# Optimization experiments

Measured on AMD Instinct MI355X. Metric: run time of the kernel, lower is better.

Reference implementation:

```python
import jax, jax.numpy as jnp
import numpy as np

B, C, T = 2, 128, 25000
OUT_C = 128
N_NODES = B * T            # 50000, nodes after flatten
N_EDGES = 800000           # avg degree 16


def setup_inputs() -> dict:
    key = jax.random.key(0)
    k1, k2, k3 = jax.random.split(key, 3)
    x = jax.random.normal(k1, (B, C, T), dtype=jnp.float32)
    W = jax.random.normal(k2, (C, OUT_C), dtype=jnp.float32) * (1.0 / np.sqrt(C))
    bias = jnp.zeros((OUT_C,), dtype=jnp.float32)
    edge_index = jax.random.randint(k3, (2, N_EDGES), 0, N_NODES, dtype=jnp.int64)
    return {"x": x, "W": W, "bias": bias, "edge_index": edge_index}


def reference(x, W, bias, edge_index):
    b, c, t = x.shape
    n = b * t
    flat = x.transpose(0, 2, 1).reshape(n, c)          # [N, C]
    h = flat @ W                                       # [N, OUT_C] transform first (GCNConv)
    src, dst = edge_index[0], edge_index[1]
    # in-degree with self-loops (PyG GCNConv default symmetric norm)
    deg = jnp.zeros((n,), dtype=h.dtype).at[dst].add(1.0) + 1.0
    dinv_sqrt = jax.lax.rsqrt(deg)
    norm = dinv_sqrt[src] * dinv_sqrt[dst]             # [E]
    msgs = h[src] * norm[:, None]                      # [E, OUT_C] gather + scale
    agg = jax.ops.segment_sum(msgs, dst, num_segments=n)
    agg = agg + h * (1.0 / deg)[:, None]               # self-loop term: norm_ii = 1/deg_i
    out = jax.nn.relu(agg + bias)
    return out.reshape(b, t, -1).transpose(0, 2, 1)    # [B, OUT_C, T]
```

## Files before the change

kernel.cpp:

```cpp
#include <hip/hip_runtime.h>

#define TT 25000
#define BB 2
#define CC 128
#define NN (BB*TT)
#define NB ((NN + 255) / 256)

typedef __attribute__((ext_vector_type(8))) short bf16x8;
typedef __attribute__((ext_vector_type(4))) float f32x4;

__device__ inline unsigned short f2bf(float f) {
    unsigned int u = __float_as_uint(f);
    u += 0x7FFF + ((u >> 16) & 1);
    return (unsigned short)(u >> 16);
}
__device__ inline float bfhi(unsigned int v) { return __uint_as_float(v << 16); }
__device__ inline float bflo(unsigned int v) { return __uint_as_float(v & 0xFFFF0000u); }

__global__ __launch_bounds__(256) void k_deg(const int* __restrict__ dst, int E,
                                             int* __restrict__ deg,
                                             int* __restrict__ eseq) {
    int i0 = blockIdx.x * 512 + threadIdx.x;
    int i1 = i0 + 256;
    int d0 = 0, d1 = 0;
    bool ok0 = (i0 < E), ok1 = (i1 < E);
    if (ok0) d0 = dst[i0];
    if (ok1) d1 = dst[i1];
    if (ok0) eseq[i0] = atomicAdd(&deg[d0], 1);
    if (ok1) eseq[i1] = atomicAdd(&deg[d1], 1);
}

__global__ __launch_bounds__(256) void k_bsum(const int* __restrict__ deg,
                                              int* __restrict__ bsum) {
    __shared__ int red[256];
    int tid = threadIdx.x;
    int i = blockIdx.x * 256 + tid;
    red[tid] = (i < NN) ? deg[i] : 0;
    __syncthreads();
#pragma unroll
    for (int o = 128; o > 0; o >>= 1) {
        if (tid < o) red[tid] += red[tid + o];
        __syncthreads();
    }
    if (tid == 0) bsum[blockIdx.x] = red[0];
}

__global__ __launch_bounds__(256) void k_scan2(const int* __restrict__ deg,
                                               const int* __restrict__ bsum,
                                               int* __restrict__ off,
                                               float* __restrict__ dinv) {
    __shared__ int part[256];
    __shared__ int bpref;
    int tid = threadIdx.x;
    int i = blockIdx.x * 256 + tid;

    part[tid] = (tid < NB && tid < blockIdx.x) ? bsum[tid] : 0;
    __syncthreads();
#pragma unroll
    for (int o = 128; o > 0; o >>= 1) {
        if (tid < o) part[tid] += part[tid + o];
        __syncthreads();
    }
    if (tid == 0) bpref = part[0];
    __syncthreads();
    int base = bpref;
    __syncthreads();

    int v = (i < NN) ? deg[i] : 0;
    part[tid] = v;
    __syncthreads();
#pragma unroll
    for (int o = 1; o < 256; o <<= 1) {
        int u = (tid >= o) ? part[tid - o] : 0;
        __syncthreads();
        part[tid] += u;
        __syncthreads();
    }
    int incl = part[tid];
    if (i < NN) {
        off[i]  = base + incl - v;
        dinv[i] = rsqrtf((float)(v + 1));
    }
    if (i == NN - 1) off[NN] = base + incl;
}

__global__ __launch_bounds__(256) void k_fill(const int* __restrict__ src,
                                              const int* __restrict__ dst, int E,
                                              const int* __restrict__ off,
                                              const int* __restrict__ eseq,
                                              int* __restrict__ csr_src) {
    int i = blockIdx.x * blockDim.x + threadIdx.x;
    if (i < E) {
        int d = dst[i];
        csr_src[off[d] + eseq[i]] = src[i];
    }
}

__global__ __launch_bounds__(256) void k_gemm(const float* __restrict__ x,
                                              const float* __restrict__ W,
                                              const float* __restrict__ dinv,
                                              unsigned short* __restrict__ h) {
    __shared__ __align__(16) unsigned short a_lds[4][4][64][8];
    __shared__ __align__(16) unsigned short b_lds[8][4][64][8];
    int tid = threadIdx.x;
    int n0 = blockIdx.x * 64;

    {
        int m = tid & 63;
        int n = n0 + m;
        bool ok = (n < NN);
        int b = 0, t = 0;
        if (ok) { b = n / TT; t = n - b * TT; }
        const float* xp = x + ((size_t)b * CC) * TT + t;
        int mt = m >> 4, lm = m & 15;
#pragma unroll
        for (int p = 0; p < 4; ++p) {
            int kg = (tid >> 6) + p * 4;
            unsigned short tmp[8];
#pragma unroll
            for (int j = 0; j < 8; ++j) {
                float v = ok ? xp[(size_t)(kg * 8 + j) * TT] : 0.f;
                tmp[j] = f2bf(v);
            }
            int kk = kg >> 2, q = kg & 3;
            *(bf16x8*)&a_lds[mt][kk][lm | (q << 4)][0] = *(bf16x8*)tmp;
        }
    }
    {
        int nc = tid & 127;
        int nt = nc >> 4, ln = nc & 15;
#pragma unroll
        for (int p = 0; p < 8; ++p) {
            int kg = (tid >> 7) + p * 2;
            unsigned short tmp[8];
#pragma unroll
            for (int j = 0; j < 8; ++j)
                tmp[j] = f2bf(W[(kg * 8 + j) * CC + nc]);
            int kk = kg >> 2, q = kg & 3;
            *(bf16x8*)&b_lds[nt][kk][ln | (q << 4)][0] = *(bf16x8*)tmp;
        }
    }
    __syncthreads();

    int lane = tid & 63;
    int w = tid >> 6;
    f32x4 acc[8];
#pragma unroll
    for (int nt = 0; nt < 8; ++nt) acc[nt] = (f32x4){0.f, 0.f, 0.f, 0.f};
#pragma unroll
    for (int kk = 0; kk < 4; ++kk) {
        bf16x8 a = *(const bf16x8*)&a_lds[w][kk][lane][0];
#pragma unroll
        for (int nt = 0; nt < 8; ++nt) {
            bf16x8 bb = *(const bf16x8*)&b_lds[nt][kk][lane][0];
            acc[nt] = __builtin_amdgcn_mfma_f32_16x16x32_bf16(a, bb, acc[nt], 0, 0, 0);
        }
    }

    int q = lane >> 4, col = lane & 15;
    int nodebase = n0 + w * 16 + q * 4;
    float di[4];
#pragma unroll
    for (int r = 0; r < 4; ++r) {
        int nn = nodebase + r;
        di[r] = (nn < NN) ? dinv[nn] : 0.f;
    }
#pragma unroll
    for (int nt = 0; nt < 8; ++nt) {
#pragma unroll
        for (int r = 0; r < 4; ++r) {
            int nn = nodebase + r;
            if (nn < NN)
                h[(size_t)nn * CC + nt * 16 + col] = f2bf(di[r] * acc[nt][r]);
        }
    }
}

__global__ __launch_bounds__(256) void k_agg(const unsigned int* __restrict__ hb,
                                             const int* __restrict__ off,
                                             const int* __restrict__ csr_src,
                                             const float* __restrict__ dinv,
                                             const float* __restrict__ bias,
                                             float* __restrict__ agg) {
    int lane = threadIdx.x & 63;
    int w    = threadIdx.x >> 6;
    int n    = blockIdx.x * 4 + w;
    if (n >= NN) return;
    float ax = 0.f, ay = 0.f;
    int e0 = off[n], e1 = off[n + 1];

    for (int c0 = e0; c0 < e1; c0 += 64) {
        int cnt = e1 - c0; if (cnt > 64) cnt = 64;
        int li = lane < cnt ? lane : cnt - 1;
        int iv = csr_src[c0 + li];
        int j = 0;
        for (; j + 16 <= cnt; j += 16) {
            int s[16];
#pragma unroll
            for (int u = 0; u < 16; ++u) s[u] = __shfl(iv, j + u, 64);
            unsigned int v[16];
#pragma unroll
            for (int u = 0; u < 16; ++u) v[u] = hb[(size_t)s[u] * 64 + lane];
#pragma unroll
            for (int u = 0; u < 16; ++u) { ax += bfhi(v[u]); ay += bflo(v[u]); }
        }
        for (; j + 4 <= cnt; j += 4) {
            int s[4];
#pragma unroll
            for (int u = 0; u < 4; ++u) s[u] = __shfl(iv, j + u, 64);
            unsigned int v[4];
#pragma unroll
            for (int u = 0; u < 4; ++u) v[u] = hb[(size_t)s[u] * 64 + lane];
#pragma unroll
            for (int u = 0; u < 4; ++u) { ax += bfhi(v[u]); ay += bflo(v[u]); }
        }
        for (; j < cnt; ++j) {
            int s = __shfl(iv, j, 64);
            unsigned int v = hb[(size_t)s * 64 + lane];
            ax += bfhi(v); ay += bflo(v);
        }
    }

    unsigned int hv = hb[(size_t)n * 64 + lane];
    ax += bfhi(hv);
    ay += bflo(hv);
    float di = dinv[n];
    const float2* b2 = (const float2*)bias;
    float2 bb = b2[lane];
    float rx = fmaxf(fmaf(di, ax, bb.x), 0.f);
    float ry = fmaxf(fmaf(di, ay, bb.y), 0.f);
    ((float2*)agg)[(size_t)n * 64 + lane] = make_float2(rx, ry);
}

__global__ void k_trans(const float* __restrict__ agg, float* __restrict__ out) {
    __shared__ float tile[32][33];
    int t0 = blockIdx.x * 32;
    int o0 = blockIdx.y * 32;
    int b  = blockIdx.z;
    int tx = threadIdx.x, ty = threadIdx.y;
#pragma unroll
    for (int i = 0; i < 4; ++i) {
        int t = t0 + ty + i * 8;
        if (t < TT) tile[ty + i * 8][tx] = agg[(size_t)(b * TT + t) * CC + o0 + tx];
    }
    __syncthreads();
#pragma unroll
    for (int i = 0; i < 4; ++i) {
        int t  = t0 + tx;
        int oc = o0 + ty + i * 8;
        if (t < TT) out[((size_t)b * CC + oc) * TT + t] = tile[tx][ty + i * 8];
    }
}

extern "C" void kernel_launch(void* const* d_in, const int* in_sizes, int n_in,
                              void* d_out, int out_size, void* d_ws, size_t ws_size,
                              hipStream_t stream) {
    const float* x    = (const float*)d_in[0];
    const float* W    = (const float*)d_in[1];
    const float* bias = (const float*)d_in[2];
    const int*   ei   = (const int*)d_in[3];
    int E = in_sizes[3] / 2;
    const int* src = ei;
    const int* dst = ei + E;
    float* out = (float*)d_out;

    char* ws = (char*)d_ws;
    size_t o = 0;
    unsigned short* h = (unsigned short*)(ws + o); o += (size_t)NN * CC * 2;
    float* agg  = (float*)(ws + o); o += (size_t)NN * CC * 4;
    int*   deg  = (int*)  (ws + o); o += (size_t)NN * 4;
    float* dinv = (float*)(ws + o); o += (size_t)NN * 4;
    int*   off  = (int*)  (ws + o); o += (size_t)(NN + 1) * 4 + 12;
    int*   bsum = (int*)  (ws + o); o += (size_t)((NB + 3) & ~3) * 4;
    int*   eseq = (int*)  (ws + o); o += (size_t)E * 4;
    int*   csrs = (int*)  (ws + o); o += (size_t)E * 4;

    hipMemsetAsync(deg, 0, (size_t)NN * 4, stream);

    k_deg  <<<(E + 511) / 512, 256, 0, stream>>>(dst, E, deg, eseq);
    k_bsum <<<NB, 256, 0, stream>>>(deg, bsum);
    k_scan2<<<NB, 256, 0, stream>>>(deg, bsum, off, dinv);
    k_fill <<<(E + 255) / 256, 256, 0, stream>>>(src, dst, E, off, eseq, csrs);
    k_gemm <<<(NN + 63) / 64, 256, 0, stream>>>(x, W, dinv, h);
    k_agg  <<<(NN + 3) / 4, 256, 0, stream>>>((const unsigned int*)h, off, csrs, dinv, bias, agg);
    dim3 tg((TT + 31) / 32, CC / 32, BB);
    k_trans<<<tg, dim3(32, 8), 0, stream>>>(agg, out);
}
```

Before: 196.6 us.

## Split node features into channel panels and aggregate per panel with bf16 intermediate

The GEMM now writes h as four 32-channel panels of 64 bytes per node. Aggregation runs in four passes, one per panel, so each pass's gather working set (about 3.2MB) can stay in L2. Within a wave, four edges are gathered at once across lane quarters and reduced with shuffles. The intermediate aggregate is stored as bf16 to halve transpose traffic, and k_deg handles four edges per thread. The cost is more launches, 64-byte gathers that fill cache lines less, and extra rounding of the output to bf16.

```diff
diff --git a/kernel.cpp b/kernel.cpp
--- a/kernel.cpp
+++ b/kernel.cpp
@@ -20,14 +20,17 @@
 __global__ __launch_bounds__(256) void k_deg(const int* __restrict__ dst, int E,
                                              int* __restrict__ deg,
                                              int* __restrict__ eseq) {
-    int i0 = blockIdx.x * 512 + threadIdx.x;
-    int i1 = i0 + 256;
-    int d0 = 0, d1 = 0;
-    bool ok0 = (i0 < E), ok1 = (i1 < E);
-    if (ok0) d0 = dst[i0];
-    if (ok1) d1 = dst[i1];
-    if (ok0) eseq[i0] = atomicAdd(&deg[d0], 1);
-    if (ok1) eseq[i1] = atomicAdd(&deg[d1], 1);
+    int base = blockIdx.x * 1024 + threadIdx.x;
+    int d[4]; bool ok[4];
+#pragma unroll
+    for (int u = 0; u < 4; ++u) {
+        int i = base + u * 256;
+        ok[u] = (i < E);
+        d[u] = ok[u] ? dst[i] : 0;
+    }
+#pragma unroll
+    for (int u = 0; u < 4; ++u)
+        if (ok[u]) eseq[base + u * 256] = atomicAdd(&deg[d[u]], 1);
 }
 
 __global__ __launch_bounds__(256) void k_bsum(const int* __restrict__ deg,
@@ -167,25 +170,29 @@
     }
 #pragma unroll
     for (int nt = 0; nt < 8; ++nt) {
+        size_t pbase = (size_t)(nt >> 1) * ((size_t)NN * 32);
 #pragma unroll
         for (int r = 0; r < 4; ++r) {
             int nn = nodebase + r;
             if (nn < NN)
-                h[(size_t)nn * CC + nt * 16 + col] = f2bf(di[r] * acc[nt][r]);
-        }
-    }
-}
-
-__global__ __launch_bounds__(256) void k_agg(const unsigned int* __restrict__ hb,
-                                             const int* __restrict__ off,
-                                             const int* __restrict__ csr_src,
-                                             const float* __restrict__ dinv,
-                                             const float* __restrict__ bias,
-                                             float* __restrict__ agg) {
+                h[pbase + (size_t)nn * 32 + (nt & 1) * 16 + col] = f2bf(di[r] * acc[nt][r]);
+        }
+    }
+}
+
+__global__ __launch_bounds__(256) void k_aggp(const unsigned int* __restrict__ hp,
+                                              const int* __restrict__ off,
+                                              const int* __restrict__ csr_src,
+                                              const float* __restrict__ dinv,
+                                              const float* __restrict__ bias,
+                                              unsigned int* __restrict__ agg16,
+                                              int pass) {
     int lane = threadIdx.x & 63;
     int w    = threadIdx.x >> 6;
     int n    = blockIdx.x * 4 + w;
     if (n >= NN) return;
+    int sub = lane & 15;
+    int quarter = lane >> 4;
     float ax = 0.f, ay = 0.f;
     int e0 = off[n], e1 = off[n + 1];
 
@@ -193,62 +200,60 @@
         int cnt = e1 - c0; if (cnt > 64) cnt = 64;
         int li = lane < cnt ? lane : cnt - 1;
         int iv = csr_src[c0 + li];
-        int j = 0;
-        for (; j + 16 <= cnt; j += 16) {
-            int s[16];
-#pragma unroll
-            for (int u = 0; u < 16; ++u) s[u] = __shfl(iv, j + u, 64);
-            unsigned int v[16];
-#pragma unroll
-            for (int u = 0; u < 16; ++u) v[u] = hb[(size_t)s[u] * 64 + lane];
-#pragma unroll
-            for (int u = 0; u < 16; ++u) { ax += bfhi(v[u]); ay += bflo(v[u]); }
-        }
-        for (; j + 4 <= cnt; j += 4) {
-            int s[4];
-#pragma unroll
-            for (int u = 0; u < 4; ++u) s[u] = __shfl(iv, j + u, 64);
-            unsigned int v[4];
-#pragma unroll
-            for (int u = 0; u < 4; ++u) v[u] = hb[(size_t)s[u] * 64 + lane];
-#pragma unroll
-            for (int u = 0; u < 4; ++u) { ax += bfhi(v[u]); ay += bflo(v[u]); }
-        }
-        for (; j < cnt; ++j) {
-            int s = __shfl(iv, j, 64);
-            unsigned int v = hb[(size_t)s * 64 + lane];
-            ax += bfhi(v); ay += bflo(v);
-        }
-    }
-
-    unsigned int hv = hb[(size_t)n * 64 + lane];
-    ax += bfhi(hv);
-    ay += bflo(hv);
+        for (int j = 0; j < cnt; j += 16) {
+            unsigned int v[4]; bool act[4];
+#pragma unroll
+            for (int u = 0; u < 4; ++u) {
+                int ei = j + u * 4 + quarter;
+                act[u] = (ei < cnt);
+                int s = __shfl(iv, act[u] ? ei : 0, 64);
+                v[u] = hp[(size_t)s * 16 + sub];
+            }
+#pragma unroll
+            for (int u = 0; u < 4; ++u) {
+                if (act[u]) { ax += bfhi(v[u]); ay += bflo(v[u]); }
+            }
+        }
+    }
+    ax += __shfl_xor(ax, 16, 64);  ay += __shfl_xor(ay, 16, 64);
+    ax += __shfl_xor(ax, 32, 64);  ay += __shfl_xor(ay, 32, 64);
+
+    unsigned int hv = hp[(size_t)n * 16 + sub];
+    ax += bfhi(hv); ay += bflo(hv);
+
     float di = dinv[n];
-    const float2* b2 = (const float2*)bias;
-    float2 bb = b2[lane];
+    float2 bb = ((const float2*)bias)[pass * 16 + sub];
     float rx = fmaxf(fmaf(di, ax, bb.x), 0.f);
     float ry = fmaxf(fmaf(di, ay, bb.y), 0.f);
-    ((float2*)agg)[(size_t)n * 64 + lane] = make_float2(rx, ry);
-}
-
-__global__ void k_trans(const float* __restrict__ agg, float* __restrict__ out) {
-    __shared__ float tile[32][33];
+    if (quarter == 0) {
+        unsigned int packed = (unsigned int)f2bf(rx) | ((unsigned int)f2bf(ry) << 16);
+        agg16[(size_t)n * 64 + pass * 16 + sub] = packed;
+    }
+}
+
+__global__ void k_trans(const unsigned int* __restrict__ agg16, float* __restrict__ out) {
+    __shared__ float tile[32][65];
     int t0 = blockIdx.x * 32;
-    int o0 = blockIdx.y * 32;
+    int p0 = blockIdx.y * 32;
     int b  = blockIdx.z;
     int tx = threadIdx.x, ty = threadIdx.y;
 #pragma unroll
     for (int i = 0; i < 4; ++i) {
         int t = t0 + ty + i * 8;
-        if (t < TT) tile[ty + i * 8][tx] = agg[(size_t)(b * TT + t) * CC + o0 + tx];
-    }
-    __syncthreads();
-#pragma unroll
-    for (int i = 0; i < 4; ++i) {
-        int t  = t0 + tx;
-        int oc = o0 + ty + i * 8;
-        if (t < TT) out[((size_t)b * CC + oc) * TT + t] = tile[tx][ty + i * 8];
+        if (t < TT) {
+            unsigned int u = agg16[(size_t)(b * TT + t) * 64 + p0 + tx];
+            tile[ty + i * 8][2 * tx]     = bfhi(u);
+            tile[ty + i * 8][2 * tx + 1] = bflo(u);
+        }
+    }
+    __syncthreads();
+    int t = t0 + tx;
+    if (t < TT) {
+#pragma unroll
+        for (int i = 0; i < 8; ++i) {
+            int ch = ty + i * 8;
+            out[((size_t)b * CC + 2 * p0 + ch) * TT + t] = tile[tx][ch];
+        }
     }
 }
 
@@ -267,7 +272,7 @@
     char* ws = (char*)d_ws;
     size_t o = 0;
     unsigned short* h = (unsigned short*)(ws + o); o += (size_t)NN * CC * 2;
-    float* agg  = (float*)(ws + o); o += (size_t)NN * CC * 4;
+    unsigned int* agg16 = (unsigned int*)(ws + o); o += (size_t)NN * 64 * 4;
     int*   deg  = (int*)  (ws + o); o += (size_t)NN * 4;
     float* dinv = (float*)(ws + o); o += (size_t)NN * 4;
     int*   off  = (int*)  (ws + o); o += (size_t)(NN + 1) * 4 + 12;
@@ -277,12 +282,15 @@
 
     hipMemsetAsync(deg, 0, (size_t)NN * 4, stream);
 
-    k_deg  <<<(E + 511) / 512, 256, 0, stream>>>(dst, E, deg, eseq);
+    k_deg  <<<(E + 1023) / 1024, 256, 0, stream>>>(dst, E, deg, eseq);
     k_bsum <<<NB, 256, 0, stream>>>(deg, bsum);
     k_scan2<<<NB, 256, 0, stream>>>(deg, bsum, off, dinv);
     k_fill <<<(E + 255) / 256, 256, 0, stream>>>(src, dst, E, off, eseq, csrs);
     k_gemm <<<(NN + 63) / 64, 256, 0, stream>>>(x, W, dinv, h);
-    k_agg  <<<(NN + 3) / 4, 256, 0, stream>>>((const unsigned int*)h, off, csrs, dinv, bias, agg);
-    dim3 tg((TT + 31) / 32, CC / 32, BB);
-    k_trans<<<tg, dim3(32, 8), 0, stream>>>(agg, out);
-}
+    for (int pass = 0; pass < 4; ++pass) {
+        const unsigned int* hp = (const unsigned int*)(h + (size_t)pass * NN * 32);
+        k_aggp<<<(NN + 3) / 4, 256, 0, stream>>>(hp, off, csrs, dinv, bias, agg16, pass);
+    }
+    dim3 tg((TT + 31) / 32, 2, BB);
+    k_trans<<<tg, dim3(32, 8), 0, stream>>>(agg16, out);
+}
```

Result: slower. 236.5 us (+20.3%).
